# Kernel tuning notes

Measured on AMD Instinct MI355X. Metric: run time of the kernel, lower is better.

## Reference

```python
import jax, jax.numpy as jnp
import numpy as np

K = 6                 # color-coding parameter; K-1 message-passing steps
N = 50000             # num nodes
E = 1600000           # num edges (avg degree 32)
F = 384               # num_node_features = K * 2**K


def setup_inputs() -> dict:
    key = jax.random.key(0)
    k1, k2, k3, k4, k5 = jax.random.split(key, 5)
    s = 1.0 / np.sqrt(F)
    x = jax.random.normal(k1, (N, F), dtype=jnp.float32)
    edge_index = jax.random.randint(k2, (2, E), 0, N, dtype=jnp.int32)
    batch = jnp.zeros((N,), dtype=jnp.int32)  # unused by forward, kept for signature parity
    W_rel = jax.random.normal(k3, (F, F), dtype=jnp.float32) * s   # GraphConv lin_rel weight
    W_root = jax.random.normal(k4, (F, F), dtype=jnp.float32) * s  # GraphConv lin_root weight
    W_lin = jax.random.normal(k5, (1, F), dtype=jnp.float32) * s   # readout linear (no bias)
    return {"x": x, "edge_index": edge_index, "batch": batch,
            "W_rel": W_rel, "W_root": W_root, "W_lin": W_lin}


def reference(x, edge_index, batch, W_rel, W_root, W_lin):
    src = edge_index[0]
    dst = edge_index[1]
    # K-1 iterations of PyG GraphConv(aggr='add', bias=False) + relu:
    #   out = segment_sum(x[src] -> dst) @ W_rel^T + x @ W_root^T
    for _ in range(K - 1):
        agg = jax.ops.segment_sum(x[src], dst, num_segments=N)  # [N, F]
        x = jax.nn.relu(agg @ W_rel.T + x @ W_root.T)
    # readout: Linear(F, 1, bias=False)
    return x @ W_lin.T  # [N, 1]
```

## Files before the change

### kernel.cpp

```cpp
#include <hip/hip_runtime.h>
#include <hip/hip_bf16.h>

#define NN 50000
#define EE 1600000
#define FF 384
#define MPAD 50048
#define NITER 5

typedef unsigned int u32;
typedef unsigned short u16;
typedef __attribute__((ext_vector_type(8))) short short8;
typedef __attribute__((ext_vector_type(4))) float f32x4;

typedef const __attribute__((address_space(1))) void* gptr_t;
typedef __attribute__((address_space(3))) void* lptr_t;

__device__ __forceinline__ float bf_lo(u32 u) {
  u32 v = u << 16;
  return __builtin_bit_cast(float, v);
}
__device__ __forceinline__ float bf_hi(u32 u) {
  u32 v = u & 0xFFFF0000u;
  return __builtin_bit_cast(float, v);
}
__device__ __forceinline__ u32 f2bf(float f) {
  u32 u = __builtin_bit_cast(u32, f);
  return (u + 0x7FFFu + ((u >> 16) & 1u)) >> 16;
}
__device__ __forceinline__ u32 pack2(float lo, float hi) {
  return f2bf(lo) | (f2bf(hi) << 16);
}
__device__ __forceinline__ void load16_lds(const void* g, void* l) {
  __builtin_amdgcn_global_load_lds((gptr_t)g, (lptr_t)l, 16, 0, 0);
}

__global__ void hist_kernel(const int* __restrict__ key, int* __restrict__ cnt) {
  int e = blockIdx.x * 256 + threadIdx.x;
  if (e < EE) atomicAdd(&cnt[key[e]], 1);
}

__global__ void scan_kernel(const int* __restrict__ cnt, int* __restrict__ row_start,
                            int* __restrict__ cursor) {
  __shared__ int wsum[4];
  const int CH = 196;
  int t = threadIdx.x;
  int lo = t * CH;
  int hi = lo + CH; if (hi > NN) hi = NN;
  int s = 0;
  int n4 = (hi - lo) >> 2;
  const int4* p = (const int4*)(cnt + lo);
  for (int i = 0; i < n4; ++i) { int4 c = p[i]; s += c.x + c.y + c.z + c.w; }
  int lane = t & 63, w = t >> 6;
  int v = s;
  for (int d = 1; d < 64; d <<= 1) { int u = __shfl_up(v, d, 64); if (lane >= d) v += u; }
  if (lane == 63) wsum[w] = v;
  __syncthreads();
  int run = v - s;
  for (int i = 0; i < w; ++i) run += wsum[i];
  int4* q1 = (int4*)(row_start + lo);
  int4* q2 = (int4*)(cursor + lo);
  for (int k = 0; k < n4; ++k) {
    int4 c = p[k];
    int4 o; o.x = run; o.y = run + c.x; o.z = o.y + c.y; o.w = o.z + c.z;
    run = o.w + c.w;
    q1[k] = o; q2[k] = o;
  }
  if (hi == NN && lo < NN) row_start[NN] = run;
}

__global__ void scatter_kernel(const int* __restrict__ src, const int* __restrict__ dst,
                               int* __restrict__ cursor, int* __restrict__ col) {
  int e = blockIdx.x * 256 + threadIdx.x;
  if (e < EE) {
    int d = dst[e];
    int p = atomicAdd(&cursor[d], 1);
    col[p] = src[e];
  }
}

__global__ void convert_x_kernel(const float* __restrict__ xin, u16* __restrict__ xout) {
  size_t i = ((size_t)blockIdx.x * 256 + threadIdx.x) * 4;
  if (i >= (size_t)NN * FF) return;
  float4 f = *(const float4*)(xin + i);
  u32 o0 = pack2(f.x, f.y);
  u32 o1 = pack2(f.z, f.w);
  u32* q = (u32*)(xout + i);
  q[0] = o0; q[1] = o1;
}

__global__ void build_bt_kernel(const float* __restrict__ Wr, const float* __restrict__ Wt,
                                u16* __restrict__ Bt) {
  int i = blockIdx.x * 256 + threadIdx.x;
  if (i >= FF * 2 * FF) return;
  int n = i / (2 * FF);
  int k = i - n * (2 * FF);
  float v = (k < FF) ? Wr[n * FF + k] : Wt[n * FF + (k - FF)];
  Bt[i] = (u16)f2bf(v);
}

__global__ void spmm_pass_kernel(const u16* __restrict__ x, const int* __restrict__ rs,
                                 const int* __restrict__ col, u16* __restrict__ agg,
                                 const int fo) {
  int row = blockIdx.x * 4 + (threadIdx.x >> 6);
  int lane = threadIdx.x & 63;
  if (row >= NN) return;
  int j0 = rs[row], j1 = rs[row + 1];
  float alo = 0.f, ahi = 0.f;
  const u32* xw = (const u32*)x + fo + lane;
  int j = j0;
  for (; j + 8 <= j1; j += 8) {
    int s0 = col[j + 0], s1 = col[j + 1], s2 = col[j + 2], s3 = col[j + 3];
    int s4 = col[j + 4], s5 = col[j + 5], s6 = col[j + 6], s7 = col[j + 7];
    u32 u0 = xw[(size_t)s0 * 192];
    u32 u1 = xw[(size_t)s1 * 192];
    u32 u2 = xw[(size_t)s2 * 192];
    u32 u3 = xw[(size_t)s3 * 192];
    u32 u4 = xw[(size_t)s4 * 192];
    u32 u5 = xw[(size_t)s5 * 192];
    u32 u6 = xw[(size_t)s6 * 192];
    u32 u7 = xw[(size_t)s7 * 192];
    alo += bf_lo(u0) + bf_lo(u1) + bf_lo(u2) + bf_lo(u3) +
           bf_lo(u4) + bf_lo(u5) + bf_lo(u6) + bf_lo(u7);
    ahi += bf_hi(u0) + bf_hi(u1) + bf_hi(u2) + bf_hi(u3) +
           bf_hi(u4) + bf_hi(u5) + bf_hi(u6) + bf_hi(u7);
  }
  for (; j < j1; ++j) {
    u32 u = xw[(size_t)col[j] * 192];
    alo += bf_lo(u); ahi += bf_hi(u);
  }
  ((u32*)agg)[(size_t)row * 192 + fo + lane] = pack2(alo, ahi);
}

__global__ __launch_bounds__(512, 4) void gemm_kernel(
    const u16* __restrict__ Aagg, const u16* __restrict__ Ax,
    const u16* __restrict__ Bt, u16* __restrict__ Xout) {
  __shared__ __align__(16) u16 As[2][64 * 64];
  __shared__ __align__(16) u16 Bs[384 * 64];

  const int orig = blockIdx.x;
  const int xcd = orig & 7, idx = orig >> 3;
  const int wg = ((xcd < 6) ? xcd * 98 : 6 * 98 + (xcd - 6) * 97) + idx;
  const int m0 = wg * 64;

  const int tid = threadIdx.x;
  const int lane = tid & 63;
  const int w = tid >> 6;
  const int wr = w >> 2;
  const int wc = w & 3;

  f32x4 acc[2][6] = {};

#define STAGE_A(KT, BUF)                                                        \
  {                                                                             \
    const u16* Asrc_ = ((KT) < 6) ? Aagg : Ax;                                  \
    const int kbA_ = (((KT) < 6) ? (KT) : (KT)-6) << 7;                         \
    const int rA_ = tid >> 3;                                                   \
    const int bcA_ = (tid & 7) << 4;                                            \
    load16_lds((const char*)Asrc_ + (size_t)(m0 + rA_) * 768 + kbA_ +           \
                   (bcA_ ^ ((rA_ & 7) << 4)),                                   \
               (char*)&As[BUF][0] + tid * 16);                                  \
  }

#define STAGE_B(KT)                                                             \
  {                                                                             \
    const int kbB_ = (KT) << 7;                                                 \
    _Pragma("unroll")                                                           \
    for (int i = 0; i < 6; ++i) {                                               \
      const int c = tid + i * 512;                                              \
      const int rB_ = c >> 3;                                                   \
      const int bcB_ = (c & 7) << 4;                                            \
      load16_lds((const char*)Bt + (size_t)rB_ * 1536 + kbB_ +                  \
                     (bcB_ ^ ((rB_ & 7) << 4)),                                 \
                 (char*)&Bs[0] + c * 16);                                       \
    }                                                                           \
  }

  STAGE_A(0, 0);
  STAGE_B(0);
  __syncthreads();

  int buf = 0;
  for (int kt = 0; kt < 12; ++kt) {
    if (kt < 11) STAGE_A(kt + 1, buf ^ 1);
#pragma unroll
    for (int ks = 0; ks < 2; ++ks) {
      short8 af[2], bfm[6];
#pragma unroll
      for (int ni = 0; ni < 6; ++ni) {
        const int r = wc * 96 + ni * 16 + (lane & 15);
        const int bc = (ks * 64 + ((lane >> 4) << 4)) ^ ((r & 7) << 4);
        bfm[ni] = *(const short8*)((const char*)&Bs[0] + r * 128 + bc);
      }
#pragma unroll
      for (int mi = 0; mi < 2; ++mi) {
        const int r = wr * 32 + mi * 16 + (lane & 15);
        const int bc = (ks * 64 + ((lane >> 4) << 4)) ^ ((r & 7) << 4);
        af[mi] = *(const short8*)((const char*)&As[buf][0] + r * 128 + bc);
      }
#pragma unroll
      for (int mi = 0; mi < 2; ++mi)
#pragma unroll
        for (int ni = 0; ni < 6; ++ni)
          acc[mi][ni] = __builtin_amdgcn_mfma_f32_16x16x32_bf16(af[mi], bfm[ni], acc[mi][ni], 0, 0, 0);
    }
    __syncthreads();
    if (kt < 11) {
      STAGE_B(kt + 1);
      __syncthreads();
    }
    buf ^= 1;
  }

#pragma unroll
  for (int mi = 0; mi < 2; ++mi) {
#pragma unroll
    for (int r = 0; r < 4; ++r) {
      const int row = m0 + wr * 32 + mi * 16 + ((lane >> 4) << 2) + r;
      u16* orow = Xout + (size_t)row * FF + wc * 96 + (lane & 15);
#pragma unroll
      for (int ni = 0; ni < 6; ++ni) {
        float v = fmaxf(acc[mi][ni][r], 0.0f);
        orow[ni * 16] = (u16)f2bf(v);
      }
    }
  }
#undef STAGE_A
#undef STAGE_B
}

__global__ void readout_kernel(const u16* __restrict__ x, const float* __restrict__ wl,
                               float* __restrict__ out) {
  int row = blockIdx.x * 4 + (threadIdx.x >> 6);
  int lane = threadIdx.x & 63;
  if (row >= NN) return;
  const u32* p = (const u32*)(x + (size_t)row * FF) + lane * 3;
  u32 u0 = p[0], u1 = p[1], u2 = p[2];
  const float* w = wl + lane * 6;
  float s = bf_lo(u0) * w[0] + bf_hi(u0) * w[1] +
            bf_lo(u1) * w[2] + bf_hi(u1) * w[3] +
            bf_lo(u2) * w[4] + bf_hi(u2) * w[5];
#pragma unroll
  for (int off = 32; off > 0; off >>= 1) s += __shfl_down(s, off, 64);
  if (lane == 0) out[row] = s;
}

extern "C" void kernel_launch(void* const* d_in, const int* in_sizes, int n_in,
                              void* d_out, int out_size, void* d_ws, size_t ws_size,
                              hipStream_t stream) {
  const float* x_in = (const float*)d_in[0];
  const int* ei = (const int*)d_in[1];
  const float* W_rel = (const float*)d_in[3];
  const float* W_root = (const float*)d_in[4];
  const float* W_lin = (const float*)d_in[5];
  float* out = (float*)d_out;

  char* ws = (char*)d_ws;
  int* cnt = (int*)(ws);
  int* row_start = (int*)(ws + 200064);
  int* cursor = (int*)(ws + 400128);
  int* col = (int*)(ws + 600192);
  u16* Bt = (u16*)(ws + 7000192);
  u16* agg = (u16*)(ws + 7590016);
  u16* x0 = (u16*)(ws + 46026880);
  u16* x1 = (u16*)(ws + 84463744);
  if (ws_size < (size_t)122900608) return;

  const int* esrc = ei;
  const int* edst = ei + EE;

  hipMemsetAsync(cnt, 0, NN * sizeof(int), stream);
  hipMemsetAsync(agg + (size_t)NN * FF, 0, (size_t)(MPAD - NN) * FF * sizeof(u16), stream);
  hipMemsetAsync(x0 + (size_t)NN * FF, 0, (size_t)(MPAD - NN) * FF * sizeof(u16), stream);
  hipMemsetAsync(x1 + (size_t)NN * FF, 0, (size_t)(MPAD - NN) * FF * sizeof(u16), stream);

  hist_kernel<<<EE / 256, 256, 0, stream>>>(edst, cnt);
  scan_kernel<<<1, 256, 0, stream>>>(cnt, row_start, cursor);
  scatter_kernel<<<EE / 256, 256, 0, stream>>>(esrc, edst, cursor, col);
  convert_x_kernel<<<(NN * FF / 4 + 255) / 256, 256, 0, stream>>>(x_in, x0);
  build_bt_kernel<<<(FF * 2 * FF + 255) / 256, 256, 0, stream>>>(W_rel, W_root, Bt);

  u16* xs = x0;
  u16* xd = x1;
  for (int t = 0; t < NITER; ++t) {
    for (int p = 0; p < 3; ++p)
      spmm_pass_kernel<<<NN / 4, 256, 0, stream>>>(xs, row_start, col, agg, p * 64);
    gemm_kernel<<<MPAD / 64, 512, 0, stream>>>(agg, xs, Bt, xd);
    u16* tmp = xs; xs = xd; xd = tmp;
  }
  readout_kernel<<<NN / 4, 256, 0, stream>>>(xs, W_lin, out);
}
```

Measured before the change: 1.265 ms.

## Fuse SpMM aggregation into GEMM kernel and partition scatter by destination range

Replaces the three per-feature-slice SpMM passes plus a separate GEMM with one fused kernel. Each 32-row block gathers neighbor rows with 16-byte loads into a swizzled LDS tile and then runs the MFMA GEMM against the W_rel/W_root weights. This removes the agg buffer's round trip through global memory and the extra launches, but the tile shrinks to 32 rows with 256 threads and uses more LDS, which may lower occupancy. The scatter kernel is also split so each group of blocks handles only one eighth of the destination range, aiming at better atomic and write locality.

```diff
diff --git a/kernel.cpp b/kernel.cpp
--- a/kernel.cpp
+++ b/kernel.cpp
@@ -68,13 +68,20 @@
   if (hi == NN && lo < NN) row_start[NN] = run;
 }
 
-__global__ void scatter_kernel(const int* __restrict__ src, const int* __restrict__ dst,
-                               int* __restrict__ cursor, int* __restrict__ col) {
-  int e = blockIdx.x * 256 + threadIdx.x;
-  if (e < EE) {
+#define SC_BLK_PER_GRP 64
+__global__ void scatter_part_kernel(const int* __restrict__ src, const int* __restrict__ dst,
+                                    int* __restrict__ cursor, int* __restrict__ col) {
+  const int g = blockIdx.x & 7;
+  const int bi = blockIdx.x >> 3;
+  const int lo = g * (NN / 8), hi = lo + (NN / 8);
+  const int chunk = EE / SC_BLK_PER_GRP;
+  const int e1 = (bi + 1) * chunk;
+  for (int e = bi * chunk + threadIdx.x; e < e1; e += 256) {
     int d = dst[e];
-    int p = atomicAdd(&cursor[d], 1);
-    col[p] = src[e];
+    if (d >= lo && d < hi) {
+      int p = atomicAdd(&cursor[d], 1);
+      col[p] = src[e];
+    }
   }
 }
 
@@ -98,75 +105,35 @@
   Bt[i] = (u16)f2bf(v);
 }
 
-__global__ void spmm_pass_kernel(const u16* __restrict__ x, const int* __restrict__ rs,
-                                 const int* __restrict__ col, u16* __restrict__ agg,
-                                 const int fo) {
-  int row = blockIdx.x * 4 + (threadIdx.x >> 6);
-  int lane = threadIdx.x & 63;
-  if (row >= NN) return;
-  int j0 = rs[row], j1 = rs[row + 1];
-  float alo = 0.f, ahi = 0.f;
-  const u32* xw = (const u32*)x + fo + lane;
-  int j = j0;
-  for (; j + 8 <= j1; j += 8) {
-    int s0 = col[j + 0], s1 = col[j + 1], s2 = col[j + 2], s3 = col[j + 3];
-    int s4 = col[j + 4], s5 = col[j + 5], s6 = col[j + 6], s7 = col[j + 7];
-    u32 u0 = xw[(size_t)s0 * 192];
-    u32 u1 = xw[(size_t)s1 * 192];
-    u32 u2 = xw[(size_t)s2 * 192];
-    u32 u3 = xw[(size_t)s3 * 192];
-    u32 u4 = xw[(size_t)s4 * 192];
-    u32 u5 = xw[(size_t)s5 * 192];
-    u32 u6 = xw[(size_t)s6 * 192];
-    u32 u7 = xw[(size_t)s7 * 192];
-    alo += bf_lo(u0) + bf_lo(u1) + bf_lo(u2) + bf_lo(u3) +
-           bf_lo(u4) + bf_lo(u5) + bf_lo(u6) + bf_lo(u7);
-    ahi += bf_hi(u0) + bf_hi(u1) + bf_hi(u2) + bf_hi(u3) +
-           bf_hi(u4) + bf_hi(u5) + bf_hi(u6) + bf_hi(u7);
-  }
-  for (; j < j1; ++j) {
-    u32 u = xw[(size_t)col[j] * 192];
-    alo += bf_lo(u); ahi += bf_hi(u);
-  }
-  ((u32*)agg)[(size_t)row * 192 + fo + lane] = pack2(alo, ahi);
-}
-
-__global__ __launch_bounds__(512, 4) void gemm_kernel(
-    const u16* __restrict__ Aagg, const u16* __restrict__ Ax,
-    const u16* __restrict__ Bt, u16* __restrict__ Xout) {
-  __shared__ __align__(16) u16 As[2][64 * 64];
+#define ACC8(u)                                  \
+  a0 += bf_lo(u.x); a1 += bf_hi(u.x);            \
+  a2 += bf_lo(u.y); a3 += bf_hi(u.y);            \
+  a4 += bf_lo(u.z); a5 += bf_hi(u.z);            \
+  a6 += bf_lo(u.w); a7 += bf_hi(u.w);
+
+__global__ __launch_bounds__(256, 2) void fused_kernel(
+    const u16* __restrict__ xs, const int* __restrict__ rs,
+    const int* __restrict__ col, const u16* __restrict__ Bt,
+    u16* __restrict__ Xout) {
+  __shared__ __align__(16) u16 Agg[32 * 384];
+  __shared__ __align__(16) u16 Axs[2][32 * 64];
   __shared__ __align__(16) u16 Bs[384 * 64];
 
   const int orig = blockIdx.x;
   const int xcd = orig & 7, idx = orig >> 3;
-  const int wg = ((xcd < 6) ? xcd * 98 : 6 * 98 + (xcd - 6) * 97) + idx;
-  const int m0 = wg * 64;
+  const int wg = ((xcd < 4) ? xcd * 196 : 4 * 196 + (xcd - 4) * 195) + idx;
+  const int m0 = wg * 32;
 
   const int tid = threadIdx.x;
   const int lane = tid & 63;
   const int w = tid >> 6;
-  const int wr = w >> 2;
-  const int wc = w & 3;
-
-  f32x4 acc[2][6] = {};
-
-#define STAGE_A(KT, BUF)                                                        \
-  {                                                                             \
-    const u16* Asrc_ = ((KT) < 6) ? Aagg : Ax;                                  \
-    const int kbA_ = (((KT) < 6) ? (KT) : (KT)-6) << 7;                         \
-    const int rA_ = tid >> 3;                                                   \
-    const int bcA_ = (tid & 7) << 4;                                            \
-    load16_lds((const char*)Asrc_ + (size_t)(m0 + rA_) * 768 + kbA_ +           \
-                   (bcA_ ^ ((rA_ & 7) << 4)),                                   \
-               (char*)&As[BUF][0] + tid * 16);                                  \
-  }
 
 #define STAGE_B(KT)                                                             \
   {                                                                             \
     const int kbB_ = (KT) << 7;                                                 \
     _Pragma("unroll")                                                           \
-    for (int i = 0; i < 6; ++i) {                                               \
-      const int c = tid + i * 512;                                              \
+    for (int i = 0; i < 12; ++i) {                                              \
+      const int c = tid + i * 256;                                              \
       const int rB_ = c >> 3;                                                   \
       const int bcB_ = (c & 7) << 4;                                            \
       load16_lds((const char*)Bt + (size_t)rB_ * 1536 + kbB_ +                  \
@@ -175,27 +142,105 @@
     }                                                                           \
   }
 
-  STAGE_A(0, 0);
+#define STAGE_AX(S, BUF)                                                        \
+  {                                                                             \
+    const int rA_ = tid >> 3;                                                   \
+    const int bcA_ = (tid & 7) << 4;                                            \
+    load16_lds((const char*)xs + (size_t)(m0 + rA_) * 768 + ((S) << 7) +        \
+                   (bcA_ ^ ((rA_ & 7) << 4)),                                   \
+               (char*)&Axs[BUF][0] + tid * 16);                                 \
+  }
+
   STAGE_B(0);
+
+  {
+    const bool active = lane < 48;
+    const int off = lane * 4;
+    for (int i = 0; i < 8; ++i) {
+      const int row = m0 + w * 8 + i;
+      float a0 = 0.f, a1 = 0.f, a2 = 0.f, a3 = 0.f;
+      float a4 = 0.f, a5 = 0.f, a6 = 0.f, a7 = 0.f;
+      if (row < NN) {
+        int j0 = rs[row], j1 = rs[row + 1];
+        int j = j0;
+        for (; j + 4 <= j1; j += 4) {
+          int s0 = col[j], s1 = col[j + 1], s2 = col[j + 2], s3 = col[j + 3];
+          if (active) {
+            uint4 u0 = *(const uint4*)((const u32*)(xs + (size_t)s0 * FF) + off);
+            uint4 u1 = *(const uint4*)((const u32*)(xs + (size_t)s1 * FF) + off);
+            uint4 u2 = *(const uint4*)((const u32*)(xs + (size_t)s2 * FF) + off);
+            uint4 u3 = *(const uint4*)((const u32*)(xs + (size_t)s3 * FF) + off);
+            ACC8(u0); ACC8(u1); ACC8(u2); ACC8(u3);
+          }
+        }
+        for (; j < j1; ++j) {
+          int s0 = col[j];
+          if (active) {
+            uint4 u0 = *(const uint4*)((const u32*)(xs + (size_t)s0 * FF) + off);
+            ACC8(u0);
+          }
+        }
+      }
+      if (active) {
+        uint4 o;
+        o.x = pack2(a0, a1); o.y = pack2(a2, a3);
+        o.z = pack2(a4, a5); o.w = pack2(a6, a7);
+        const int rl = w * 8 + i;
+        const int b = lane * 16;
+        char* p = (char*)&Agg[0] + rl * 768 + (b & ~127) + ((b & 127) ^ ((rl & 7) << 4));
+        *(uint4*)p = o;
+      }
+    }
+  }
   __syncthreads();
 
-  int buf = 0;
-  for (int kt = 0; kt < 12; ++kt) {
-    if (kt < 11) STAGE_A(kt + 1, buf ^ 1);
+  f32x4 acc[2][6] = {};
+
+  for (int kt = 0; kt < 6; ++kt) {
+    if (kt == 5) STAGE_AX(0, 0);
 #pragma unroll
     for (int ks = 0; ks < 2; ++ks) {
       short8 af[2], bfm[6];
 #pragma unroll
       for (int ni = 0; ni < 6; ++ni) {
-        const int r = wc * 96 + ni * 16 + (lane & 15);
+        const int r = w * 96 + ni * 16 + (lane & 15);
         const int bc = (ks * 64 + ((lane >> 4) << 4)) ^ ((r & 7) << 4);
         bfm[ni] = *(const short8*)((const char*)&Bs[0] + r * 128 + bc);
       }
 #pragma unroll
       for (int mi = 0; mi < 2; ++mi) {
-        const int r = wr * 32 + mi * 16 + (lane & 15);
+        const int r = mi * 16 + (lane & 15);
+        const int inner = (ks * 64 + ((lane >> 4) << 4)) ^ ((r & 7) << 4);
+        af[mi] = *(const short8*)((const char*)&Agg[0] + r * 768 + kt * 128 + inner);
+      }
+#pragma unroll
+      for (int mi = 0; mi < 2; ++mi)
+#pragma unroll
+        for (int ni = 0; ni < 6; ++ni)
+          acc[mi][ni] = __builtin_amdgcn_mfma_f32_16x16x32_bf16(af[mi], bfm[ni], acc[mi][ni], 0, 0, 0);
+    }
+    __syncthreads();
+    STAGE_B(kt + 1);
+    __syncthreads();
+  }
+
+  int buf = 0;
+  for (int kt = 6; kt < 12; ++kt) {
+    if (kt < 11) STAGE_AX(kt - 5, buf ^ 1);
+#pragma unroll
+    for (int ks = 0; ks < 2; ++ks) {
+      short8 af[2], bfm[6];
+#pragma unroll
+      for (int ni = 0; ni < 6; ++ni) {
+        const int r = w * 96 + ni * 16 + (lane & 15);
         const int bc = (ks * 64 + ((lane >> 4) << 4)) ^ ((r & 7) << 4);
-        af[mi] = *(const short8*)((const char*)&As[buf][0] + r * 128 + bc);
+        bfm[ni] = *(const short8*)((const char*)&Bs[0] + r * 128 + bc);
+      }
+#pragma unroll
+      for (int mi = 0; mi < 2; ++mi) {
+        const int r = mi * 16 + (lane & 15);
+        const int inner = (ks * 64 + ((lane >> 4) << 4)) ^ ((r & 7) << 4);
+        af[mi] = *(const short8*)((const char*)&Axs[buf][0] + r * 128 + inner);
       }
 #pragma unroll
       for (int mi = 0; mi < 2; ++mi)
@@ -215,8 +260,8 @@
   for (int mi = 0; mi < 2; ++mi) {
 #pragma unroll
     for (int r = 0; r < 4; ++r) {
-      const int row = m0 + wr * 32 + mi * 16 + ((lane >> 4) << 2) + r;
-      u16* orow = Xout + (size_t)row * FF + wc * 96 + (lane & 15);
+      const int row = m0 + mi * 16 + ((lane >> 4) << 2) + r;
+      u16* orow = Xout + (size_t)row * FF + w * 96 + (lane & 15);
 #pragma unroll
       for (int ni = 0; ni < 6; ++ni) {
         float v = fmaxf(acc[mi][ni][r], 0.0f);
@@ -224,8 +269,8 @@
       }
     }
   }
-#undef STAGE_A
 #undef STAGE_B
+#undef STAGE_AX
 }
 
 __global__ void readout_kernel(const u16* __restrict__ x, const float* __restrict__ wl,
@@ -260,7 +305,6 @@
   int* cursor = (int*)(ws + 400128);
   int* col = (int*)(ws + 600192);
   u16* Bt = (u16*)(ws + 7000192);
-  u16* agg = (u16*)(ws + 7590016);
   u16* x0 = (u16*)(ws + 46026880);
   u16* x1 = (u16*)(ws + 84463744);
   if (ws_size < (size_t)122900608) return;
@@ -269,22 +313,19 @@
   const int* edst = ei + EE;
 
   hipMemsetAsync(cnt, 0, NN * sizeof(int), stream);
-  hipMemsetAsync(agg + (size_t)NN * FF, 0, (size_t)(MPAD - NN) * FF * sizeof(u16), stream);
   hipMemsetAsync(x0 + (size_t)NN * FF, 0, (size_t)(MPAD - NN) * FF * sizeof(u16), stream);
   hipMemsetAsync(x1 + (size_t)NN * FF, 0, (size_t)(MPAD - NN) * FF * sizeof(u16), stream);
 
   hist_kernel<<<EE / 256, 256, 0, stream>>>(edst, cnt);
   scan_kernel<<<1, 256, 0, stream>>>(cnt, row_start, cursor);
-  scatter_kernel<<<EE / 256, 256, 0, stream>>>(esrc, edst, cursor, col);
+  scatter_part_kernel<<<8 * SC_BLK_PER_GRP, 256, 0, stream>>>(esrc, edst, cursor, col);
   convert_x_kernel<<<(NN * FF / 4 + 255) / 256, 256, 0, stream>>>(x_in, x0);
   build_bt_kernel<<<(FF * 2 * FF + 255) / 256, 256, 0, stream>>>(W_rel, W_root, Bt);
 
   u16* xs = x0;
   u16* xd = x1;
   for (int t = 0; t < NITER; ++t) {
-    for (int p = 0; p < 3; ++p)
-      spmm_pass_kernel<<<NN / 4, 256, 0, stream>>>(xs, row_start, col, agg, p * 64);
-    gemm_kernel<<<MPAD / 64, 512, 0, stream>>>(agg, xs, Bt, xd);
+    fused_kernel<<<MPAD / 32, 256, 0, stream>>>(xs, row_start, col, Bt, xd);
     u16* tmp = xs; xs = xd; xd = tmp;
   }
   readout_kernel<<<NN / 4, 256, 0, stream>>>(xs, W_lin, out);
```

Result: slower. 1.746 ms (+38.1%).

## Pre-bucket edges by destination range before CSR scatter for locality

Applied to the files above, without the earlier changes.

Replaces the single atomic scatter that builds CSR column indices with two passes. The first pass sorts each chunk of edges into 8 destination-range buckets in LDS and writes them out contiguously. The second pass does the per-node cursor atomics bucket by bucket, so the atomics and column writes stay within a smaller address range with better cache locality. This adds an extra kernel launch and an extra read and write of the edge arrays, and it relies on fixed bucket capacities being large enough for the random edge distribution.

```diff
diff --git a/kernel.cpp b/kernel.cpp
--- a/kernel.cpp
+++ b/kernel.cpp
@@ -6,6 +6,8 @@
 #define FF 384
 #define MPAD 50048
 #define NITER 5
+#define EPB 6250
+#define BCAP 220000
 
 typedef unsigned int u32;
 typedef unsigned short u16;
@@ -40,10 +42,11 @@
 }
 
 __global__ void scan_kernel(const int* __restrict__ cnt, int* __restrict__ row_start,
-                            int* __restrict__ cursor) {
+                            int* __restrict__ cursor, int* __restrict__ bcur) {
   __shared__ int wsum[4];
   const int CH = 196;
   int t = threadIdx.x;
+  if (t < 8) bcur[t] = t * BCAP;
   int lo = t * CH;
   int hi = lo + CH; if (hi > NN) hi = NN;
   int s = 0;
@@ -68,13 +71,53 @@
   if (hi == NN && lo < NN) row_start[NN] = run;
 }
 
-__global__ void scatter_kernel(const int* __restrict__ src, const int* __restrict__ dst,
-                               int* __restrict__ cursor, int* __restrict__ col) {
-  int e = blockIdx.x * 256 + threadIdx.x;
-  if (e < EE) {
-    int d = dst[e];
+__global__ __launch_bounds__(256) void bucket_scatter_kernel(
+    const int* __restrict__ src, const int* __restrict__ dst,
+    int* __restrict__ bcur, int* __restrict__ es_src, int* __restrict__ es_dst) {
+  __shared__ int osrc[EPB];
+  __shared__ int odst[EPB];
+  __shared__ int h[8], lo8[8], gbase[8], c2[8];
+  const int t = threadIdx.x;
+  if (t < 8) { h[t] = 0; c2[t] = 0; }
+  __syncthreads();
+  const int e0 = blockIdx.x * EPB;
+  for (int i = t; i < EPB; i += 256) {
+    int d = dst[e0 + i];
+    atomicAdd(&h[d / 6250], 1);
+  }
+  __syncthreads();
+  if (t == 0) { int r = 0; for (int b = 0; b < 8; ++b) { lo8[b] = r; r += h[b]; } }
+  __syncthreads();
+  if (t < 8) gbase[t] = atomicAdd(&bcur[t], h[t]);
+  __syncthreads();
+  for (int i = t; i < EPB; i += 256) {
+    int s = src[e0 + i], d = dst[e0 + i];
+    int b = d / 6250;
+    int p = lo8[b] + atomicAdd(&c2[b], 1);
+    osrc[p] = s; odst[p] = d;
+  }
+  __syncthreads();
+  for (int i = t; i < EPB; i += 256) {
+    int b = 0;
+    while (b < 7 && i >= lo8[b + 1]) ++b;
+    int g = gbase[b] + (i - lo8[b]);
+    es_src[g] = osrc[i];
+    es_dst[g] = odst[i];
+  }
+}
+
+__global__ void scatter_final_kernel(const int* __restrict__ es_src,
+                                     const int* __restrict__ es_dst,
+                                     const int* __restrict__ bcur,
+                                     int* __restrict__ cursor, int* __restrict__ col) {
+  const int g = blockIdx.x & 7;
+  const int bi = blockIdx.x >> 3;
+  const int base = g * BCAP;
+  const int cnt = bcur[g] - base;
+  for (int i = bi * 256 + threadIdx.x; i < cnt; i += 64 * 256) {
+    int d = es_dst[base + i];
     int p = atomicAdd(&cursor[d], 1);
-    col[p] = src[e];
+    col[p] = es_src[base + i];
   }
 }
 
@@ -256,6 +299,7 @@
 
   char* ws = (char*)d_ws;
   int* cnt = (int*)(ws);
+  int* bcur = cnt + NN;
   int* row_start = (int*)(ws + 200064);
   int* cursor = (int*)(ws + 400128);
   int* col = (int*)(ws + 600192);
@@ -264,6 +308,8 @@
   u16* x0 = (u16*)(ws + 46026880);
   u16* x1 = (u16*)(ws + 84463744);
   if (ws_size < (size_t)122900608) return;
+  int* es_src = (int*)(ws + 7590016);
+  int* es_dst = (int*)(ws + 7590016 + 7040000);
 
   const int* esrc = ei;
   const int* edst = ei + EE;
@@ -274,8 +320,9 @@
   hipMemsetAsync(x1 + (size_t)NN * FF, 0, (size_t)(MPAD - NN) * FF * sizeof(u16), stream);
 
   hist_kernel<<<EE / 256, 256, 0, stream>>>(edst, cnt);
-  scan_kernel<<<1, 256, 0, stream>>>(cnt, row_start, cursor);
-  scatter_kernel<<<EE / 256, 256, 0, stream>>>(esrc, edst, cursor, col);
+  scan_kernel<<<1, 256, 0, stream>>>(cnt, row_start, cursor, bcur);
+  bucket_scatter_kernel<<<EE / EPB, 256, 0, stream>>>(esrc, edst, bcur, es_src, es_dst);
+  scatter_final_kernel<<<512, 256, 0, stream>>>(es_src, es_dst, bcur, cursor, col);
   convert_x_kernel<<<(NN * FF / 4 + 255) / 256, 256, 0, stream>>>(x_in, x0);
   build_bt_kernel<<<(FF * 2 * FF + 255) / 256, 256, 0, stream>>>(W_rel, W_root, Bt);
 
```

New measurement: 1.240 ms. Within noise of the previous version (-1.9%).
